# Kernel optimization log

Measured on AMD Instinct MI355X. Metric: run time of the kernel, lower is better.

Reference implementation:

```python
import math
import jax, jax.numpy as jnp
import numpy as np

NUM_HEADS = 32
NUM_KV_HEADS = 8
HEAD_SIZE = 128
FEATURE_DIM = 64
SEQ_LEN = 2048
WINDOW_SIZE = 64
EPS = 1e-12
MASK_VALUE = -100000000.0


def _make_masks(n: int, w: int):
    # block-diagonal ones(w,w) tiles, plus the rolled (sub-diagonal) tiles
    m = math.ceil(n / w)
    mask = np.kron(np.eye(m), np.ones((w, w)))
    mask = mask + np.roll(mask, -w, axis=-1)
    mask = mask[:n, :n]
    mask_window = np.tril(mask).astype(bool)[None, None]          # [1,1,n,n]
    mask_linear = np.tril(1.0 - mask).astype(bool)[None, None]    # [1,1,n,n]
    return jnp.asarray(mask_window), jnp.asarray(mask_linear)


def _feature_map(w, x):
    # f(x) = clamp(cat(softmax(xW), softmax(-xW)), min=eps)
    z = jnp.einsum('hdf,bhld->bhlf', w, x)
    return jnp.clip(
        jnp.concatenate([jax.nn.softmax(z, axis=-1), jax.nn.softmax(-z, axis=-1)], axis=-1),
        EPS, None)


def setup_inputs() -> dict:
    key = jax.random.key(0)
    ks = jax.random.split(key, 6)
    return {
        'query': jax.random.normal(ks[0], (SEQ_LEN, NUM_HEADS * HEAD_SIZE), dtype=jnp.float32),
        'key': jax.random.normal(ks[1], (SEQ_LEN, NUM_KV_HEADS * HEAD_SIZE), dtype=jnp.float32),
        'value': jax.random.normal(ks[2], (SEQ_LEN, NUM_KV_HEADS * HEAD_SIZE), dtype=jnp.float32),
        'fmap_q_w': 0.02 * jax.random.normal(ks[3], (NUM_HEADS, HEAD_SIZE, FEATURE_DIM), dtype=jnp.float32),
        'fmap_k_w': 0.02 * jax.random.normal(ks[4], (NUM_HEADS, HEAD_SIZE, FEATURE_DIM), dtype=jnp.float32),
        'window_factors': jax.random.normal(ks[5], (1, NUM_HEADS, 1, 1), dtype=jnp.float32),
    }


def reference(query, key, value, fmap_q_w, fmap_k_w, window_factors):
    T = query.shape[0]
    q = query.reshape(T, NUM_HEADS, HEAD_SIZE)
    k = key.reshape(T, NUM_KV_HEADS, HEAD_SIZE)
    v = value.reshape(T, NUM_KV_HEADS, HEAD_SIZE)
    rep = NUM_HEADS // NUM_KV_HEADS
    k = jnp.repeat(k, rep, axis=1)
    v = jnp.repeat(v, rep, axis=1)
    # [T,H,D] -> [1,H,T,D]
    q = jnp.moveaxis(q, 0, -2)[None]
    k = jnp.moveaxis(k, 0, -2)[None]
    v = jnp.moveaxis(v, 0, -2)[None]

    f_q = _feature_map(fmap_q_w, q)  # [1,H,T,2F]
    f_k = _feature_map(fmap_k_w, k)
    wf = jax.nn.sigmoid(window_factors)

    mask_window, mask_linear = _make_masks(SEQ_LEN, WINDOW_SIZE)
    mask_window = mask_window[:, :, :T, :T]
    mask_linear = mask_linear[:, :, :T, :T]

    # sliding-window softmax term
    a_sm = jnp.einsum('bhmd,bhnd->bhmn', q, k) * (HEAD_SIZE ** -0.5)
    a_sm = jnp.where(mask_window, a_sm, MASK_VALUE)
    a_sm_max = jnp.max(a_sm, axis=-1, keepdims=True)
    a_sm = wf * jnp.exp(a_sm - a_sm_max)
    sum_sm = jnp.sum(a_sm, axis=-1, keepdims=True)

    # linear feature-map term (linear_factor = 1)
    a_ln = jnp.einsum('bhmd,bhnd->bhmn', f_q, f_k)
    a_ln = jnp.where(mask_linear, a_ln, 0.0)
    sum_ln = jnp.sum(a_ln, axis=-1, keepdims=True)

    y = jnp.einsum('bhmn,bhnd->bhmd', a_sm + a_ln, v)
    return y / (sum_sm + sum_ln)
```

## Files before the change

kernel.cpp:

```cpp
#include <hip/hip_runtime.h>
#include <math.h>

#define T_SEQ 2048
#define NH    32
#define NKV   8
#define HS    128
#define FD    64
#define NBLK  32
#define SCAN_NB 30
#define EPSF  1e-12f
#define LDP   136
#define STP   129

typedef unsigned short u16;
typedef __bf16 bf16x8 __attribute__((ext_vector_type(8)));
typedef float  f32x4  __attribute__((ext_vector_type(4)));

__device__ __forceinline__ u16 f2b(float f) {
  unsigned u = __builtin_bit_cast(unsigned, f);
  return (u16)((u + 0x7fffu + ((u >> 16) & 1u)) >> 16);
}

#define FKT_OFF 0
#define ST_OFF  16777216
#define VT_OFF  54525952
#define WT_OFF  58720256
#define KB_OFF  59768832

__device__ __forceinline__ void stage_bf(u16* buf, const u16* __restrict__ src, int tid) {
#pragma unroll
  for (int i = 0; i < 4; ++i) {
    int idx = tid * 8 + i * 2048, rr = idx >> 7, c = idx & 127;
    *(uint4*)(buf + rr * LDP + c) = *(const uint4*)(src + idx);
  }
}
__device__ __forceinline__ void stage_vt(u16* buf, const u16* __restrict__ vts,
                                         int rofs, int kb0, int B, int tid) {
#pragma unroll
  for (int i = 0; i < 4; ++i) {
    int idx = tid * 8 + i * 2048, rr = idx >> 7, c = idx & 127;
    int key = (c < 64) ? (kb0 * 64 + c) : (B * 64 + (c - 64));
    *(uint4*)(buf + rr * LDP + c) = *(const uint4*)(vts + (size_t)(rr + rofs) * T_SEQ + key);
  }
}

__global__ __launch_bounds__(256) void k_pre(
    const float* __restrict__ wq, const float* __restrict__ wk,
    const float* __restrict__ vg,
    u16* __restrict__ WT, u16* __restrict__ VT)
{
  __shared__ float sB[128 * 68];
  const int bx = blockIdx.x, tid = threadIdx.x;

  if (bx < 64) {
    const int h = bx >> 1, isk = bx & 1;
    const float* src = (isk ? wk : wq) + (size_t)h * HS * FD;
    for (int idx = tid * 4; idx < 8192; idx += 1024) {
      int r = idx >> 6, c = idx & 63;
      *(float4*)(sB + r * 68 + c) = *(const float4*)(src + idx);
    }
    __syncthreads();
    u16* dst = WT + ((size_t)(isk * NH + h)) * 8192;
    for (int i = 0; i < 8; ++i) {
      int ch = tid + i * 256;
      int f = ch >> 5, d4 = (ch & 31) * 4;
      ushort4 u;
      u.x = f2b(sB[(d4 + 0) * 68 + f]);
      u.y = f2b(sB[(d4 + 1) * 68 + f]);
      u.z = f2b(sB[(d4 + 2) * 68 + f]);
      u.w = f2b(sB[(d4 + 3) * 68 + f]);
      *(ushort4*)(dst + f * 128 + d4) = u;
    }
  } else {
    const int idx2 = bx - 64;
    const int b = idx2 & 31, kvh = idx2 >> 5;
    float* sV = sB;
    for (int idx = tid * 4; idx < 8192; idx += 1024) {
      int r = idx >> 7, c = idx & 127;
      *(float4*)(sV + r * 129 + c) = *(const float4*)(vg + (size_t)(b * 64 + r) * (NKV * HS) + kvh * HS + c);
    }
    __syncthreads();
    const int lane = tid & 63, w = tid >> 6;
#pragma unroll
    for (int i = 0; i < 32; ++i) {
      int d = w * 32 + i;
      VT[((size_t)(kvh * 128 + d)) * T_SEQ + b * 64 + lane] = f2b(sV[lane * 129 + d]);
    }
  }
}

__global__ __launch_bounds__(256) void k_fmap(
    const float* __restrict__ kg, const u16* __restrict__ WT,
    u16* __restrict__ FKT, u16* __restrict__ KBB)
{
  __shared__ __align__(16) u16 smem[2 * 64 * 136];
  u16* sX = smem;
  u16* sW = smem + 64 * 136;
  const int lt = blockIdx.x, h = blockIdx.y;
  const int tid = threadIdx.x, lane = tid & 63, w = tid >> 6;
  const int quad = lane >> 4, txn = lane & 15;

  const float* xbase = kg + (h >> 2) * HS;
  const int    xstr  = NKV * HS;
  for (int idx = tid * 4; idx < 8192; idx += 1024) {
    int r = idx >> 7, c = idx & 127;
    float4 v4 = *(const float4*)(xbase + (size_t)(lt * 64 + r) * xstr + c);
    ushort4 u; u.x = f2b(v4.x); u.y = f2b(v4.y); u.z = f2b(v4.z); u.w = f2b(v4.w);
    *(ushort4*)(sX + r * 136 + c) = u;
  }
  const u16* wt = WT + ((size_t)(NH + h)) * 8192;
  for (int i = 0; i < 4; ++i) {
    int ch = tid + i * 256;
    int row = ch >> 4, d8 = (ch & 15) * 8;
    *(uint4*)(sW + row * 136 + d8) = *(const uint4*)(wt + row * 128 + d8);
  }
  __syncthreads();

  if ((h & 3) == 0) {
    u16* ob = KBB + ((size_t)((h >> 2) * NBLK + lt)) * 8192;
    for (int i = 0; i < 4; ++i) {
      int ch = tid + i * 256;
      int row = ch >> 4, d8 = (ch & 15) * 8;
      *(uint4*)(ob + row * 128 + d8) = *(const uint4*)(sX + row * 136 + d8);
    }
  }

  const int arow = w * 16 + txn;
  const f32x4 vzero = {0.f, 0.f, 0.f, 0.f};
  f32x4 zt[4] = {vzero, vzero, vzero, vzero};
#pragma unroll
  for (int ks = 0; ks < 4; ++ks) {
    bf16x8 a = *(const bf16x8*)(sX + arow * 136 + ks * 32 + quad * 8);
#pragma unroll
    for (int nt = 0; nt < 4; ++nt) {
      bf16x8 bb = *(const bf16x8*)(sW + (nt * 16 + txn) * 136 + ks * 32 + quad * 8);
      zt[nt] = __builtin_amdgcn_mfma_f32_16x16x32_bf16(a, bb, zt[nt], 0, 0, 0);
    }
  }

  float E1[4][4], E2[4][4];
#pragma unroll
  for (int r = 0; r < 4; ++r) {
    float zv[4];
    float mx = -1e30f, mn = 1e30f;
#pragma unroll
    for (int nt = 0; nt < 4; ++nt) {
      zv[nt] = zt[nt][r];
      mx = fmaxf(mx, zv[nt]); mn = fminf(mn, zv[nt]);
    }
#pragma unroll
    for (int o = 1; o < 16; o <<= 1) {
      mx = fmaxf(mx, __shfl_xor(mx, o));
      mn = fminf(mn, __shfl_xor(mn, o));
    }
    float e1[4], e2[4], s1 = 0.f, s2 = 0.f;
#pragma unroll
    for (int nt = 0; nt < 4; ++nt) {
      e1[nt] = __expf(zv[nt] - mx); s1 += e1[nt];
      e2[nt] = __expf(mn - zv[nt]); s2 += e2[nt];
    }
#pragma unroll
    for (int o = 1; o < 16; o <<= 1) { s1 += __shfl_xor(s1, o); s2 += __shfl_xor(s2, o); }
    float r1 = 1.f / s1, r2 = 1.f / s2;
#pragma unroll
    for (int nt = 0; nt < 4; ++nt) {
      E1[r][nt] = fmaxf(e1[nt] * r1, EPSF);
      E2[r][nt] = fmaxf(e2[nt] * r2, EPSF);
    }
  }

  __syncthreads();

#pragma unroll
  for (int r = 0; r < 4; ++r) {
    int j = w * 16 + quad * 4 + r;
#pragma unroll
    for (int nt = 0; nt < 4; ++nt) {
      sX[(nt * 16 + txn) * 68 + j]        = f2b(E1[r][nt]);
      sX[(nt * 16 + txn + 64) * 68 + j]   = f2b(E2[r][nt]);
    }
  }
  __syncthreads();
  u16* ob = FKT + (size_t)h * 128 * T_SEQ + lt * 64;
  for (int i = 0; i < 8; ++i) {
    int ch = tid + i * 256;
    int row = ch >> 4, j4 = (ch & 15) * 4;
    *(ushort4*)(ob + (size_t)row * T_SEQ + j4) = *(const ushort4*)(sX + row * 68 + j4);
  }
}

__global__ __launch_bounds__(256) void k_scan(
    const u16* __restrict__ FKT, const u16* __restrict__ VT, u16* __restrict__ ST)
{
  __shared__ __align__(16) u16 sVT[16 * 72];
  __shared__ __align__(16) u16 sFK[64 * 72];
  const int L = blockIdx.x + 8 * blockIdx.y + 16 * blockIdx.z;
  const int xcd = L & 7, j = L >> 3;
  const int hsub = j & 3, fh = (j >> 2) & 1, dc = j >> 3;
  const int h = xcd * 4 + hsub;
  const int tid = threadIdx.x, lane = tid & 63, w = tid >> 6;
  const int quad = lane >> 4, txn = lane & 15;
  const bool doz = (dc == 0);

  bf16x8 vone;
#pragma unroll
  for (int jj = 0; jj < 8; ++jj) vone[jj] = (__bf16)1.0f;

  const u16* vbase = VT + ((size_t)((h >> 2) * 128 + dc * 16)) * T_SEQ;
  const u16* fbase = FKT + ((size_t)(h * 128 + fh * 64)) * T_SEQ;

  const int srow = tid >> 4, sj4 = (tid & 15) * 4;
  ushort4 rv, rf[4];
  rv = *(const ushort4*)(vbase + (size_t)srow * T_SEQ + sj4);
#pragma unroll
  for (int i = 0; i < 4; ++i) {
    int ch = tid + i * 256;
    int fr = ch >> 4, fj4 = (ch & 15) * 4;
    rf[i] = *(const ushort4*)(fbase + (size_t)fr * T_SEQ + fj4);
  }

  const f32x4 vzero = {0.f, 0.f, 0.f, 0.f};
  f32x4 acc = vzero, zacc = vzero;

  for (int b = 0; b < SCAN_NB; ++b) {
    __syncthreads();
    *(ushort4*)(sVT + srow * 72 + sj4) = rv;
#pragma unroll
    for (int i = 0; i < 4; ++i) {
      int ch = tid + i * 256;
      int fr = ch >> 4, fj4 = (ch & 15) * 4;
      *(ushort4*)(sFK + fr * 72 + fj4) = rf[i];
    }
    __syncthreads();
    if (b + 1 < SCAN_NB) {
      rv = *(const ushort4*)(vbase + (size_t)srow * T_SEQ + (b + 1) * 64 + sj4);
#pragma unroll
      for (int i = 0; i < 4; ++i) {
        int ch = tid + i * 256;
        int fr = ch >> 4, fj4 = (ch & 15) * 4;
        rf[i] = *(const ushort4*)(fbase + (size_t)fr * T_SEQ + (b + 1) * 64 + fj4);
      }
    }
#pragma unroll
    for (int ks = 0; ks < 2; ++ks) {
      bf16x8 a  = *(const bf16x8*)(sVT + txn * 72 + ks * 32 + quad * 8);
      bf16x8 bb = *(const bf16x8*)(sFK + (w * 16 + txn) * 72 + ks * 32 + quad * 8);
      acc = __builtin_amdgcn_mfma_f32_16x16x32_bf16(a, bb, acc, 0, 0, 0);
      if (doz) zacc = __builtin_amdgcn_mfma_f32_16x16x32_bf16(vone, bb, zacc, 0, 0, 0);
    }
    u16* Sb = ST + (((size_t)(h * NBLK + b)) * STP + dc * 16) * 128 + fh * 64;
#pragma unroll
    for (int r = 0; r < 4; ++r)
      Sb[(quad * 4 + r) * 128 + w * 16 + txn] = f2b(acc[r]);
    if (doz && quad == 0)
      ST[(((size_t)(h * NBLK + b)) * STP + 128) * 128 + fh * 64 + w * 16 + txn] = f2b(zacc[0]);
  }
}

__global__ __launch_bounds__(256, 4) void k_main(
    const float* __restrict__ qg, const u16* __restrict__ KBB,
    const u16* __restrict__ WT, const u16* __restrict__ ST,
    const u16* __restrict__ VT, const float* __restrict__ wfac,
    float* __restrict__ out)
{
  __shared__ __align__(16) u16 RA[64 * LDP];
  __shared__ __align__(16) u16 RB[64 * LDP];
  __shared__ __align__(16) u16 sz[128];
  const int L = blockIdx.x + 32 * blockIdx.y;
  const int xcd = L & 7, j = L >> 3;
  const int hsub = j & 3, B = j >> 2;
  const int h = xcd * 4 + hsub;
  const int tid = threadIdx.x;
  const int lane = tid & 63, w = tid >> 6;
  const int quad = lane >> 4, txn = lane & 15;
  const int arow = w * 16 + txn;
  const int koff = quad * 8;

  const f32x4 vzero = {0.f, 0.f, 0.f, 0.f};
  f32x4 y[8];
#pragma unroll
  for (int t = 0; t < 8; ++t) y[t] = vzero;
  float sln[4] = {0.f, 0.f, 0.f, 0.f};
  const bf16x8 bzero = {0, 0, 0, 0, 0, 0, 0, 0};

  const int kb0 = (B >= 1) ? B - 1 : 0;
  const u16* ktB   = KBB + ((size_t)((h >> 2) * NBLK + B)) * 8192;
  const u16* ktP   = KBB + ((size_t)((h >> 2) * NBLK + kb0)) * 8192;
  const u16* vts   = VT  + (size_t)((h >> 2) * 128) * T_SEQ;

  for (int idx = tid * 4; idx < 8192; idx += 1024) {
    int r = idx >> 7, c = idx & 127;
    float4 v4 = *(const float4*)(qg + (size_t)(B * 64 + r) * (NH * HS) + h * HS + c);
    ushort4 u; u.x = f2b(v4.x); u.y = f2b(v4.y); u.z = f2b(v4.z); u.w = f2b(v4.w);
    *(ushort4*)(RA + r * LDP + c) = u;
  }
  if (B >= 2) stage_bf(RB, WT + (size_t)h * 8192, tid);
  __syncthreads();

  f32x4 zt[4] = {vzero, vzero, vzero, vzero};
  if (B >= 2) {
#pragma unroll
    for (int ks = 0; ks < 4; ++ks) {
      bf16x8 a = *(const bf16x8*)(RA + arow * LDP + ks * 32 + koff);
#pragma unroll
      for (int nt = 0; nt < 4; ++nt) {
        bf16x8 bb = *(const bf16x8*)(RB + (nt * 16 + txn) * LDP + ks * 32 + koff);
        zt[nt] = __builtin_amdgcn_mfma_f32_16x16x32_bf16(a, bb, zt[nt], 0, 0, 0);
      }
    }
  }
  __syncthreads();
  stage_bf(RB, ktB, tid);

  unsigned Epk[4][4];
  if (B >= 2) {
#pragma unroll
    for (int r = 0; r < 4; ++r) {
      float zv[4];
      float mx = -1e30f, mn = 1e30f;
#pragma unroll
      for (int nt = 0; nt < 4; ++nt) {
        zv[nt] = zt[nt][r];
        mx = fmaxf(mx, zv[nt]); mn = fminf(mn, zv[nt]);
      }
#pragma unroll
      for (int o = 1; o < 16; o <<= 1) {
        mx = fmaxf(mx, __shfl_xor(mx, o));
        mn = fminf(mn, __shfl_xor(mn, o));
      }
      float e1[4], e2[4], s1 = 0.f, s2 = 0.f;
#pragma unroll
      for (int nt = 0; nt < 4; ++nt) {
        e1[nt] = __expf(zv[nt] - mx); s1 += e1[nt];
        e2[nt] = __expf(mn - zv[nt]); s2 += e2[nt];
      }
#pragma unroll
      for (int o = 1; o < 16; o <<= 1) { s1 += __shfl_xor(s1, o); s2 += __shfl_xor(s2, o); }
      float r1 = 1.f / s1, r2 = 1.f / s2;
#pragma unroll
      for (int nt = 0; nt < 4; ++nt) {
        unsigned lo = f2b(fmaxf(e1[nt] * r1, EPSF));
        unsigned hi = f2b(fmaxf(e2[nt] * r2, EPSF));
        Epk[r][nt] = lo | (hi << 16);
      }
    }
  }
  __syncthreads();

  f32x4 s[8];
#pragma unroll
  for (int t = 0; t < 8; ++t) s[t] = vzero;
#pragma unroll
  for (int ks = 0; ks < 4; ++ks) {
    bf16x8 a = *(const bf16x8*)(RA + arow * LDP + ks * 32 + koff);
#pragma unroll
    for (int t = 0; t < 4; ++t) {
      bf16x8 bb = *(const bf16x8*)(RB + (t * 16 + txn) * LDP + ks * 32 + koff);
      s[4 + t] = __builtin_amdgcn_mfma_f32_16x16x32_bf16(a, bb, s[4 + t], 0, 0, 0);
    }
  }

  if (B >= 1) {
    __syncthreads();
    stage_bf(RB, ktP, tid);
    __syncthreads();
#pragma unroll
    for (int ks = 0; ks < 4; ++ks) {
      bf16x8 a = *(const bf16x8*)(RA + arow * LDP + ks * 32 + koff);
#pragma unroll
      for (int t = 0; t < 4; ++t) {
        bf16x8 bb = *(const bf16x8*)(RB + (t * 16 + txn) * LDP + ks * 32 + koff);
        s[t] = __builtin_amdgcn_mfma_f32_16x16x32_bf16(a, bb, s[t], 0, 0, 0);
      }
    }
  }

  float wf = wfac[h];
  wf = 1.f / (1.f + __expf(-wf));
  const float scale = 0.08838834764831845f;
  float ssum[4];
#pragma unroll
  for (int r = 0; r < 4; ++r) {
    const int irow = w * 16 + quad * 4 + r;
    float sv[8];
    float m = -1e30f;
#pragma unroll
    for (int t = 0; t < 8; ++t) {
      float x = s[t][r] * scale;
      bool msk = (t < 4) ? (B == 0) : ((t - 4) * 16 + txn > irow);
      x = msk ? -1e30f : x;
      sv[t] = x;
      m = fmaxf(m, x);
    }
#pragma unroll
    for (int o = 1; o < 16; o <<= 1) m = fmaxf(m, __shfl_xor(m, o));
    float ss = 0.f;
#pragma unroll
    for (int t = 0; t < 8; ++t) {
      float e = (sv[t] > -1e29f) ? wf * __expf(sv[t] - m) : 0.f;
      ss += e;
      RA[irow * LDP + t * 16 + txn] = f2b(e);
    }
#pragma unroll
    for (int o = 1; o < 16; o <<= 1) ss += __shfl_xor(ss, o);
    ssum[r] = ss;
  }
  __syncthreads();

  stage_vt(RB, vts, 0, kb0, B, tid);
  __syncthreads();
#pragma unroll
  for (int ks = 0; ks < 4; ++ks) {
    if (B == 0 && ks < 2) continue;
    bf16x8 a = *(const bf16x8*)(RA + arow * LDP + ks * 32 + koff);
#pragma unroll
    for (int t = 0; t < 4; ++t) {
      bf16x8 bb = *(const bf16x8*)(RB + (t * 16 + txn) * LDP + ks * 32 + koff);
      y[t] = __builtin_amdgcn_mfma_f32_16x16x32_bf16(a, bb, y[t], 0, 0, 0);
    }
  }
  __syncthreads();

  stage_vt(RB, vts, 64, kb0, B, tid);
  __syncthreads();
#pragma unroll
  for (int ks = 0; ks < 4; ++ks) {
    if (B == 0 && ks < 2) continue;
    bf16x8 a = *(const bf16x8*)(RA + arow * LDP + ks * 32 + koff);
#pragma unroll
    for (int t = 4; t < 8; ++t) {
      bf16x8 bb = *(const bf16x8*)(RB + (t * 16 + txn - 64) * LDP + ks * 32 + koff);
      y[t] = __builtin_amdgcn_mfma_f32_16x16x32_bf16(a, bb, y[t], 0, 0, 0);
    }
  }

  if (B >= 2) {
    __syncthreads();
#pragma unroll
    for (int r = 0; r < 4; ++r) {
      int row = w * 16 + quad * 4 + r;
#pragma unroll
      for (int nt = 0; nt < 4; ++nt) {
        RA[row * LDP + nt * 16 + txn]      = (u16)(Epk[r][nt] & 0xffffu);
        RA[row * LDP + 64 + nt * 16 + txn] = (u16)(Epk[r][nt] >> 16);
      }
    }
    const u16* ssrc = ST + ((size_t)(h * NBLK + (B - 2))) * (STP * 128);
    stage_bf(RB, ssrc, tid);
    if (tid < 32) *(ushort4*)(sz + tid * 4) = *(const ushort4*)(ssrc + 16384 + tid * 4);
    __syncthreads();
    f32x4 yz = vzero;
#pragma unroll
    for (int ks = 0; ks < 4; ++ks) {
      bf16x8 a = *(const bf16x8*)(RA + arow * LDP + ks * 32 + koff);
#pragma unroll
      for (int t = 0; t < 4; ++t) {
        bf16x8 bb = *(const bf16x8*)(RB + (t * 16 + txn) * LDP + ks * 32 + koff);
        y[t] = __builtin_amdgcn_mfma_f32_16x16x32_bf16(a, bb, y[t], 0, 0, 0);
      }
      bf16x8 bz = (txn == 0) ? *(const bf16x8*)(sz + ks * 32 + koff) : bzero;
      yz = __builtin_amdgcn_mfma_f32_16x16x32_bf16(a, bz, yz, 0, 0, 0);
    }
    __syncthreads();
    stage_bf(RB, ssrc + 8192, tid);
    __syncthreads();
#pragma unroll
    for (int ks = 0; ks < 4; ++ks) {
      bf16x8 a = *(const bf16x8*)(RA + arow * LDP + ks * 32 + koff);
#pragma unroll
      for (int t = 4; t < 8; ++t) {
        bf16x8 bb = *(const bf16x8*)(RB + (t * 16 + txn - 64) * LDP + ks * 32 + koff);
        y[t] = __builtin_amdgcn_mfma_f32_16x16x32_bf16(a, bb, y[t], 0, 0, 0);
      }
    }
#pragma unroll
    for (int r = 0; r < 4; ++r) sln[r] = __shfl(yz[r], lane & 48);
  }

  const size_t obase = ((size_t)h * T_SEQ + B * 64) * HS;
#pragma unroll
  for (int r = 0; r < 4; ++r) {
    float inv = 1.f / (ssum[r] + sln[r]);
    int irow = w * 16 + quad * 4 + r;
#pragma unroll
    for (int t = 0; t < 8; ++t)
      out[obase + (size_t)irow * HS + t * 16 + txn] = y[t][r] * inv;
  }
}

extern "C" void kernel_launch(void* const* d_in, const int* in_sizes, int n_in,
                              void* d_out, int out_size, void* d_ws, size_t ws_size,
                              hipStream_t stream) {
  const float* q    = (const float*)d_in[0];
  const float* k    = (const float*)d_in[1];
  const float* v    = (const float*)d_in[2];
  const float* wq   = (const float*)d_in[3];
  const float* wk   = (const float*)d_in[4];
  const float* wfac = (const float*)d_in[5];
  float* out = (float*)d_out;
  char* wsb = (char*)d_ws;

  u16* FKT = (u16*)(wsb + FKT_OFF);
  u16* ST  = (u16*)(wsb + ST_OFF);
  u16* VT  = (u16*)(wsb + VT_OFF);
  u16* WT  = (u16*)(wsb + WT_OFF);
  u16* KBB = (u16*)(wsb + KB_OFF);

  k_pre  <<<dim3(320),      256, 0, stream>>>(wq, wk, v, WT, VT);
  k_fmap <<<dim3(NBLK, NH), 256, 0, stream>>>(k, WT, FKT, KBB);
  k_scan <<<dim3(8, 2, NH), 256, 0, stream>>>(FKT, VT, ST);
  k_main <<<dim3(NBLK, NH), 256, 0, stream>>>(q, KBB, WT, ST, VT, wfac, out);
}
```

Before: 161.5 us.

## Load MFMA operands directly from global memory, dropping LDS staging and barriers

k_main and k_scan now read the B operands (K blocks, W, V transposes, scan states) directly from global/L2 into MFMA fragments instead of staging them through shared memory behind __syncthreads. Each wave converts its own Q rows into LDS, which removes the block-wide barriers before the first MFMAs. The V transpose moves from k_pre into the k_fmap launch, so k_pre now only handles the weights. The goal is less LDS traffic and fewer barriers, at the cost of redundant, less coalesced global loads across waves.

Measured after the change: 193.2 us. 19.6% more time.

```diff
diff --git a/kernel.cpp b/kernel.cpp
--- a/kernel.cpp
+++ b/kernel.cpp
@@ -27,78 +27,62 @@
 #define WT_OFF  58720256
 #define KB_OFF  59768832
 
-__device__ __forceinline__ void stage_bf(u16* buf, const u16* __restrict__ src, int tid) {
-#pragma unroll
-  for (int i = 0; i < 4; ++i) {
-    int idx = tid * 8 + i * 2048, rr = idx >> 7, c = idx & 127;
-    *(uint4*)(buf + rr * LDP + c) = *(const uint4*)(src + idx);
-  }
-}
-__device__ __forceinline__ void stage_vt(u16* buf, const u16* __restrict__ vts,
-                                         int rofs, int kb0, int B, int tid) {
-#pragma unroll
-  for (int i = 0; i < 4; ++i) {
-    int idx = tid * 8 + i * 2048, rr = idx >> 7, c = idx & 127;
-    int key = (c < 64) ? (kb0 * 64 + c) : (B * 64 + (c - 64));
-    *(uint4*)(buf + rr * LDP + c) = *(const uint4*)(vts + (size_t)(rr + rofs) * T_SEQ + key);
-  }
-}
-
 __global__ __launch_bounds__(256) void k_pre(
     const float* __restrict__ wq, const float* __restrict__ wk,
-    const float* __restrict__ vg,
-    u16* __restrict__ WT, u16* __restrict__ VT)
+    u16* __restrict__ WT)
 {
   __shared__ float sB[128 * 68];
   const int bx = blockIdx.x, tid = threadIdx.x;
-
-  if (bx < 64) {
-    const int h = bx >> 1, isk = bx & 1;
-    const float* src = (isk ? wk : wq) + (size_t)h * HS * FD;
-    for (int idx = tid * 4; idx < 8192; idx += 1024) {
-      int r = idx >> 6, c = idx & 63;
-      *(float4*)(sB + r * 68 + c) = *(const float4*)(src + idx);
-    }
-    __syncthreads();
-    u16* dst = WT + ((size_t)(isk * NH + h)) * 8192;
-    for (int i = 0; i < 8; ++i) {
-      int ch = tid + i * 256;
-      int f = ch >> 5, d4 = (ch & 31) * 4;
-      ushort4 u;
-      u.x = f2b(sB[(d4 + 0) * 68 + f]);
-      u.y = f2b(sB[(d4 + 1) * 68 + f]);
-      u.z = f2b(sB[(d4 + 2) * 68 + f]);
-      u.w = f2b(sB[(d4 + 3) * 68 + f]);
-      *(ushort4*)(dst + f * 128 + d4) = u;
-    }
-  } else {
-    const int idx2 = bx - 64;
-    const int b = idx2 & 31, kvh = idx2 >> 5;
-    float* sV = sB;
+  const int h = bx >> 1, isk = bx & 1;
+  const float* src = (isk ? wk : wq) + (size_t)h * HS * FD;
+  for (int idx = tid * 4; idx < 8192; idx += 1024) {
+    int r = idx >> 6, c = idx & 63;
+    *(float4*)(sB + r * 68 + c) = *(const float4*)(src + idx);
+  }
+  __syncthreads();
+  u16* dst = WT + ((size_t)(isk * NH + h)) * 8192;
+  for (int i = 0; i < 8; ++i) {
+    int ch = tid + i * 256;
+    int f = ch >> 5, d4 = (ch & 31) * 4;
+    ushort4 u;
+    u.x = f2b(sB[(d4 + 0) * 68 + f]);
+    u.y = f2b(sB[(d4 + 1) * 68 + f]);
+    u.z = f2b(sB[(d4 + 2) * 68 + f]);
+    u.w = f2b(sB[(d4 + 3) * 68 + f]);
+    *(ushort4*)(dst + f * 128 + d4) = u;
+  }
+}
+
+__global__ __launch_bounds__(256) void k_fmap(
+    const float* __restrict__ kg, const float* __restrict__ vg,
+    const u16* __restrict__ WT,
+    u16* __restrict__ FKT, u16* __restrict__ KBB, u16* __restrict__ VT)
+{
+  __shared__ __align__(16) u16 smem[2 * 64 * 136];
+  const int bx = blockIdx.x;
+  const int tid = threadIdx.x, lane = tid & 63, w = tid >> 6;
+  const int quad = lane >> 4, txn = lane & 15;
+
+  if (bx < 256) {
+    const int b = bx & 31, kvh = bx >> 5;
+    float* sV = (float*)smem;
     for (int idx = tid * 4; idx < 8192; idx += 1024) {
       int r = idx >> 7, c = idx & 127;
       *(float4*)(sV + r * 129 + c) = *(const float4*)(vg + (size_t)(b * 64 + r) * (NKV * HS) + kvh * HS + c);
     }
     __syncthreads();
-    const int lane = tid & 63, w = tid >> 6;
 #pragma unroll
     for (int i = 0; i < 32; ++i) {
       int d = w * 32 + i;
       VT[((size_t)(kvh * 128 + d)) * T_SEQ + b * 64 + lane] = f2b(sV[lane * 129 + d]);
     }
-  }
-}
-
-__global__ __launch_bounds__(256) void k_fmap(
-    const float* __restrict__ kg, const u16* __restrict__ WT,
-    u16* __restrict__ FKT, u16* __restrict__ KBB)
-{
-  __shared__ __align__(16) u16 smem[2 * 64 * 136];
+    return;
+  }
+
+  const int id = bx - 256;
+  const int lt = id & 31, h = id >> 5;
   u16* sX = smem;
   u16* sW = smem + 64 * 136;
-  const int lt = blockIdx.x, h = blockIdx.y;
-  const int tid = threadIdx.x, lane = tid & 63, w = tid >> 6;
-  const int quad = lane >> 4, txn = lane & 15;
 
   const float* xbase = kg + (h >> 2) * HS;
   const int    xstr  = NKV * HS;
@@ -192,8 +176,6 @@
 __global__ __launch_bounds__(256) void k_scan(
     const u16* __restrict__ FKT, const u16* __restrict__ VT, u16* __restrict__ ST)
 {
-  __shared__ __align__(16) u16 sVT[16 * 72];
-  __shared__ __align__(16) u16 sFK[64 * 72];
   const int L = blockIdx.x + 8 * blockIdx.y + 16 * blockIdx.z;
   const int xcd = L & 7, j = L >> 3;
   const int hsub = j & 3, fh = (j >> 2) & 1, dc = j >> 3;
@@ -206,47 +188,24 @@
 #pragma unroll
   for (int jj = 0; jj < 8; ++jj) vone[jj] = (__bf16)1.0f;
 
-  const u16* vbase = VT + ((size_t)((h >> 2) * 128 + dc * 16)) * T_SEQ;
-  const u16* fbase = FKT + ((size_t)(h * 128 + fh * 64)) * T_SEQ;
-
-  const int srow = tid >> 4, sj4 = (tid & 15) * 4;
-  ushort4 rv, rf[4];
-  rv = *(const ushort4*)(vbase + (size_t)srow * T_SEQ + sj4);
-#pragma unroll
-  for (int i = 0; i < 4; ++i) {
-    int ch = tid + i * 256;
-    int fr = ch >> 4, fj4 = (ch & 15) * 4;
-    rf[i] = *(const ushort4*)(fbase + (size_t)fr * T_SEQ + fj4);
-  }
+  const u16* va = VT  + ((size_t)((h >> 2) * 128 + dc * 16 + txn)) * T_SEQ + quad * 8;
+  const u16* fa = FKT + ((size_t)(h * 128 + fh * 64 + w * 16 + txn)) * T_SEQ + quad * 8;
 
   const f32x4 vzero = {0.f, 0.f, 0.f, 0.f};
   f32x4 acc = vzero, zacc = vzero;
 
+#pragma unroll 2
   for (int b = 0; b < SCAN_NB; ++b) {
-    __syncthreads();
-    *(ushort4*)(sVT + srow * 72 + sj4) = rv;
-#pragma unroll
-    for (int i = 0; i < 4; ++i) {
-      int ch = tid + i * 256;
-      int fr = ch >> 4, fj4 = (ch & 15) * 4;
-      *(ushort4*)(sFK + fr * 72 + fj4) = rf[i];
-    }
-    __syncthreads();
-    if (b + 1 < SCAN_NB) {
-      rv = *(const ushort4*)(vbase + (size_t)srow * T_SEQ + (b + 1) * 64 + sj4);
-#pragma unroll
-      for (int i = 0; i < 4; ++i) {
-        int ch = tid + i * 256;
-        int fr = ch >> 4, fj4 = (ch & 15) * 4;
-        rf[i] = *(const ushort4*)(fbase + (size_t)fr * T_SEQ + (b + 1) * 64 + fj4);
-      }
-    }
-#pragma unroll
-    for (int ks = 0; ks < 2; ++ks) {
-      bf16x8 a  = *(const bf16x8*)(sVT + txn * 72 + ks * 32 + quad * 8);
-      bf16x8 bb = *(const bf16x8*)(sFK + (w * 16 + txn) * 72 + ks * 32 + quad * 8);
-      acc = __builtin_amdgcn_mfma_f32_16x16x32_bf16(a, bb, acc, 0, 0, 0);
-      if (doz) zacc = __builtin_amdgcn_mfma_f32_16x16x32_bf16(vone, bb, zacc, 0, 0, 0);
+    const int c0 = b * 64;
+    bf16x8 a0  = *(const bf16x8*)(va + c0);
+    bf16x8 b0  = *(const bf16x8*)(fa + c0);
+    bf16x8 a1  = *(const bf16x8*)(va + c0 + 32);
+    bf16x8 b1  = *(const bf16x8*)(fa + c0 + 32);
+    acc = __builtin_amdgcn_mfma_f32_16x16x32_bf16(a0, b0, acc, 0, 0, 0);
+    acc = __builtin_amdgcn_mfma_f32_16x16x32_bf16(a1, b1, acc, 0, 0, 0);
+    if (doz) {
+      zacc = __builtin_amdgcn_mfma_f32_16x16x32_bf16(vone, b0, zacc, 0, 0, 0);
+      zacc = __builtin_amdgcn_mfma_f32_16x16x32_bf16(vone, b1, zacc, 0, 0, 0);
     }
     u16* Sb = ST + (((size_t)(h * NBLK + b)) * STP + dc * 16) * 128 + fh * 64;
 #pragma unroll
@@ -264,11 +223,9 @@
     float* __restrict__ out)
 {
   __shared__ __align__(16) u16 RA[64 * LDP];
-  __shared__ __align__(16) u16 RB[64 * LDP];
-  __shared__ __align__(16) u16 sz[128];
   const int L = blockIdx.x + 32 * blockIdx.y;
-  const int xcd = L & 7, j = L >> 3;
-  const int hsub = j & 3, B = j >> 2;
+  const int xcd = L & 7, jj = L >> 3;
+  const int hsub = jj & 3, B = jj >> 2;
   const int h = xcd * 4 + hsub;
   const int tid = threadIdx.x;
   const int lane = tid & 63, w = tid >> 6;
@@ -284,18 +241,23 @@
   const bf16x8 bzero = {0, 0, 0, 0, 0, 0, 0, 0};
 
   const int kb0 = (B >= 1) ? B - 1 : 0;
-  const u16* ktB   = KBB + ((size_t)((h >> 2) * NBLK + B)) * 8192;
-  const u16* ktP   = KBB + ((size_t)((h >> 2) * NBLK + kb0)) * 8192;
-  const u16* vts   = VT  + (size_t)((h >> 2) * 128) * T_SEQ;
-
-  for (int idx = tid * 4; idx < 8192; idx += 1024) {
-    int r = idx >> 7, c = idx & 127;
-    float4 v4 = *(const float4*)(qg + (size_t)(B * 64 + r) * (NH * HS) + h * HS + c);
-    ushort4 u; u.x = f2b(v4.x); u.y = f2b(v4.y); u.z = f2b(v4.z); u.w = f2b(v4.w);
-    *(ushort4*)(RA + r * LDP + c) = u;
-  }
-  if (B >= 2) stage_bf(RB, WT + (size_t)h * 8192, tid);
-  __syncthreads();
+  const u16* ktB = KBB + ((size_t)((h >> 2) * NBLK + B)) * 8192;
+  const u16* ktP = KBB + ((size_t)((h >> 2) * NBLK + kb0)) * 8192;
+  const u16* vts = VT  + (size_t)((h >> 2) * 128) * T_SEQ;
+  const u16* wqt = WT  + (size_t)h * 8192;
+  const u16* ssrc = ST + ((size_t)(h * NBLK + (B >= 2 ? B - 2 : 0))) * (STP * 128);
+
+  {
+    const float* qb = qg + (size_t)(B * 64 + w * 16) * (NH * HS) + h * HS;
+#pragma unroll
+    for (int i = 0; i < 8; ++i) {
+      int idx = lane + i * 64;
+      int r = idx >> 5, c4 = (idx & 31) * 4;
+      float4 v4 = *(const float4*)(qb + (size_t)r * (NH * HS) + c4);
+      ushort4 u; u.x = f2b(v4.x); u.y = f2b(v4.y); u.z = f2b(v4.z); u.w = f2b(v4.w);
+      *(ushort4*)(RA + (w * 16 + r) * LDP + c4) = u;
+    }
+  }
 
   f32x4 zt[4] = {vzero, vzero, vzero, vzero};
   if (B >= 2) {
@@ -304,13 +266,11 @@
       bf16x8 a = *(const bf16x8*)(RA + arow * LDP + ks * 32 + koff);
 #pragma unroll
       for (int nt = 0; nt < 4; ++nt) {
-        bf16x8 bb = *(const bf16x8*)(RB + (nt * 16 + txn) * LDP + ks * 32 + koff);
+        bf16x8 bb = *(const bf16x8*)(wqt + (nt * 16 + txn) * 128 + ks * 32 + koff);
         zt[nt] = __builtin_amdgcn_mfma_f32_16x16x32_bf16(a, bb, zt[nt], 0, 0, 0);
       }
     }
   }
-  __syncthreads();
-  stage_bf(RB, ktB, tid);
 
   unsigned Epk[4][4];
   if (B >= 2) {
@@ -345,7 +305,6 @@
       }
     }
   }
-  __syncthreads();
 
   f32x4 s[8];
 #pragma unroll
@@ -355,21 +314,17 @@
     bf16x8 a = *(const bf16x8*)(RA + arow * LDP + ks * 32 + koff);
 #pragma unroll
     for (int t = 0; t < 4; ++t) {
-      bf16x8 bb = *(const bf16x8*)(RB + (t * 16 + txn) * LDP + ks * 32 + koff);
+      bf16x8 bb = *(const bf16x8*)(ktB + (t * 16 + txn) * 128 + ks * 32 + koff);
       s[4 + t] = __builtin_amdgcn_mfma_f32_16x16x32_bf16(a, bb, s[4 + t], 0, 0, 0);
     }
   }
-
   if (B >= 1) {
-    __syncthreads();
-    stage_bf(RB, ktP, tid);
-    __syncthreads();
 #pragma unroll
     for (int ks = 0; ks < 4; ++ks) {
       bf16x8 a = *(const bf16x8*)(RA + arow * LDP + ks * 32 + koff);
 #pragma unroll
       for (int t = 0; t < 4; ++t) {
-        bf16x8 bb = *(const bf16x8*)(RB + (t * 16 + txn) * LDP + ks * 32 + koff);
+        bf16x8 bb = *(const bf16x8*)(ktP + (t * 16 + txn) * 128 + ks * 32 + koff);
         s[t] = __builtin_amdgcn_mfma_f32_16x16x32_bf16(a, bb, s[t], 0, 0, 0);
       }
     }
@@ -405,37 +360,20 @@
     for (int o = 1; o < 16; o <<= 1) ss += __shfl_xor(ss, o);
     ssum[r] = ss;
   }
-  __syncthreads();
-
-  stage_vt(RB, vts, 0, kb0, B, tid);
-  __syncthreads();
+
 #pragma unroll
   for (int ks = 0; ks < 4; ++ks) {
     if (B == 0 && ks < 2) continue;
+    const int kcol = (ks < 2) ? (kb0 * 64 + ks * 32) : (B * 64 + (ks - 2) * 32);
     bf16x8 a = *(const bf16x8*)(RA + arow * LDP + ks * 32 + koff);
 #pragma unroll
-    for (int t = 0; t < 4; ++t) {
-      bf16x8 bb = *(const bf16x8*)(RB + (t * 16 + txn) * LDP + ks * 32 + koff);
+    for (int t = 0; t < 8; ++t) {
+      bf16x8 bb = *(const bf16x8*)(vts + (size_t)(t * 16 + txn) * T_SEQ + kcol + koff);
       y[t] = __builtin_amdgcn_mfma_f32_16x16x32_bf16(a, bb, y[t], 0, 0, 0);
     }
   }
-  __syncthreads();
-
-  stage_vt(RB, vts, 64, kb0, B, tid);
-  __syncthreads();
-#pragma unroll
-  for (int ks = 0; ks < 4; ++ks) {
-    if (B == 0 && ks < 2) continue;
-    bf16x8 a = *(const bf16x8*)(RA + arow * LDP + ks * 32 + koff);
-#pragma unroll
-    for (int t = 4; t < 8; ++t) {
-      bf16x8 bb = *(const bf16x8*)(RB + (t * 16 + txn - 64) * LDP + ks * 32 + koff);
-      y[t] = __builtin_amdgcn_mfma_f32_16x16x32_bf16(a, bb, y[t], 0, 0, 0);
-    }
-  }
 
   if (B >= 2) {
-    __syncthreads();
 #pragma unroll
     for (int r = 0; r < 4; ++r) {
       int row = w * 16 + quad * 4 + r;
@@ -445,33 +383,17 @@
         RA[row * LDP + 64 + nt * 16 + txn] = (u16)(Epk[r][nt] >> 16);
       }
     }
-    const u16* ssrc = ST + ((size_t)(h * NBLK + (B - 2))) * (STP * 128);
-    stage_bf(RB, ssrc, tid);
-    if (tid < 32) *(ushort4*)(sz + tid * 4) = *(const ushort4*)(ssrc + 16384 + tid * 4);
-    __syncthreads();
     f32x4 yz = vzero;
 #pragma unroll
     for (int ks = 0; ks < 4; ++ks) {
       bf16x8 a = *(const bf16x8*)(RA + arow * LDP + ks * 32 + koff);
 #pragma unroll
-      for (int t = 0; t < 4; ++t) {
-        bf16x8 bb = *(const bf16x8*)(RB + (t * 16 + txn) * LDP + ks * 32 + koff);
+      for (int t = 0; t < 8; ++t) {
+        bf16x8 bb = *(const bf16x8*)(ssrc + (t * 16 + txn) * 128 + ks * 32 + koff);
         y[t] = __builtin_amdgcn_mfma_f32_16x16x32_bf16(a, bb, y[t], 0, 0, 0);
       }
-      bf16x8 bz = (txn == 0) ? *(const bf16x8*)(sz + ks * 32 + koff) : bzero;
+      bf16x8 bz = (txn == 0) ? *(const bf16x8*)(ssrc + 16384 + ks * 32 + koff) : bzero;
       yz = __builtin_amdgcn_mfma_f32_16x16x32_bf16(a, bz, yz, 0, 0, 0);
-    }
-    __syncthreads();
-    stage_bf(RB, ssrc + 8192, tid);
-    __syncthreads();
-#pragma unroll
-    for (int ks = 0; ks < 4; ++ks) {
-      bf16x8 a = *(const bf16x8*)(RA + arow * LDP + ks * 32 + koff);
-#pragma unroll
-      for (int t = 4; t < 8; ++t) {
-        bf16x8 bb = *(const bf16x8*)(RB + (t * 16 + txn - 64) * LDP + ks * 32 + koff);
-        y[t] = __builtin_amdgcn_mfma_f32_16x16x32_bf16(a, bb, y[t], 0, 0, 0);
-      }
     }
 #pragma unroll
     for (int r = 0; r < 4; ++r) sln[r] = __shfl(yz[r], lane & 48);
@@ -506,8 +428,8 @@
   u16* WT  = (u16*)(wsb + WT_OFF);
   u16* KBB = (u16*)(wsb + KB_OFF);
 
-  k_pre  <<<dim3(320),      256, 0, stream>>>(wq, wk, v, WT, VT);
-  k_fmap <<<dim3(NBLK, NH), 256, 0, stream>>>(k, WT, FKT, KBB);
+  k_pre  <<<dim3(64),       256, 0, stream>>>(wq, wk, WT);
+  k_fmap <<<dim3(1280),     256, 0, stream>>>(k, v, WT, FKT, KBB, VT);
   k_scan <<<dim3(8, 2, NH), 256, 0, stream>>>(FKT, VT, ST);
   k_main <<<dim3(NBLK, NH), 256, 0, stream>>>(q, KBB, WT, ST, VT, wfac, out);
 }
```

## Software-pipeline global tile loads through registers and use lighter barriers in k_main

Applied to the files above, without the earlier changes.

Restructures k_main so that each global tile (K blocks, V^T halves, state halves) is loaded into registers one stage ahead and written to shared memory after the next barrier, overlapping global latency with the MFMA work. The W^T feature-map weights are now read directly from global memory instead of being staged, and each wave converts only its own Q rows, which removes the first barriers. __syncthreads is replaced with raw s_barrier, plus lgkmcnt waits where shared writes must be visible. The cost is higher register pressure from the prefetch buffer, and B<2 blocks now perform unconditional state-tile loads and barriers.

Result: slower. 165.3 us (+2.3%).

```diff
diff --git a/kernel.cpp b/kernel.cpp
--- a/kernel.cpp
+++ b/kernel.cpp
@@ -21,26 +21,37 @@
   return (u16)((u + 0x7fffu + ((u >> 16) & 1u)) >> 16);
 }
 
+__device__ __forceinline__ void bar() {
+  asm volatile("s_barrier" ::: "memory");
+}
+__device__ __forceinline__ void bar_lgkm() {
+  asm volatile("s_waitcnt lgkmcnt(0)\n\ts_barrier" ::: "memory");
+}
+
 #define FKT_OFF 0
 #define ST_OFF  16777216
 #define VT_OFF  54525952
 #define WT_OFF  58720256
 #define KB_OFF  59768832
 
-__device__ __forceinline__ void stage_bf(u16* buf, const u16* __restrict__ src, int tid) {
-#pragma unroll
-  for (int i = 0; i < 4; ++i) {
-    int idx = tid * 8 + i * 2048, rr = idx >> 7, c = idx & 127;
-    *(uint4*)(buf + rr * LDP + c) = *(const uint4*)(src + idx);
-  }
-}
-__device__ __forceinline__ void stage_vt(u16* buf, const u16* __restrict__ vts,
-                                         int rofs, int kb0, int B, int tid) {
+__device__ __forceinline__ void ld_tile(uint4 p[4], const u16* __restrict__ src, int tid) {
+#pragma unroll
+  for (int i = 0; i < 4; ++i) p[i] = *(const uint4*)(src + tid * 8 + i * 2048);
+}
+__device__ __forceinline__ void ld_vt(uint4 p[4], const u16* __restrict__ vts,
+                                      int rofs, int kb0, int B, int tid) {
 #pragma unroll
   for (int i = 0; i < 4; ++i) {
     int idx = tid * 8 + i * 2048, rr = idx >> 7, c = idx & 127;
     int key = (c < 64) ? (kb0 * 64 + c) : (B * 64 + (c - 64));
-    *(uint4*)(buf + rr * LDP + c) = *(const uint4*)(vts + (size_t)(rr + rofs) * T_SEQ + key);
+    p[i] = *(const uint4*)(vts + (size_t)(rr + rofs) * T_SEQ + key);
+  }
+}
+__device__ __forceinline__ void wr_tile(u16* buf, int tid, const uint4 p[4]) {
+#pragma unroll
+  for (int i = 0; i < 4; ++i) {
+    int idx = tid * 8 + i * 2048, rr = idx >> 7, c = idx & 127;
+    *(uint4*)(buf + rr * LDP + c) = p[i];
   }
 }
 
@@ -223,7 +234,7 @@
   f32x4 acc = vzero, zacc = vzero;
 
   for (int b = 0; b < SCAN_NB; ++b) {
-    __syncthreads();
+    bar();
     *(ushort4*)(sVT + srow * 72 + sj4) = rv;
 #pragma unroll
     for (int i = 0; i < 4; ++i) {
@@ -231,7 +242,7 @@
       int fr = ch >> 4, fj4 = (ch & 15) * 4;
       *(ushort4*)(sFK + fr * 72 + fj4) = rf[i];
     }
-    __syncthreads();
+    bar_lgkm();
     if (b + 1 < SCAN_NB) {
       rv = *(const ushort4*)(vbase + (size_t)srow * T_SEQ + (b + 1) * 64 + sj4);
 #pragma unroll
@@ -267,8 +278,8 @@
   __shared__ __align__(16) u16 RB[64 * LDP];
   __shared__ __align__(16) u16 sz[128];
   const int L = blockIdx.x + 32 * blockIdx.y;
-  const int xcd = L & 7, j = L >> 3;
-  const int hsub = j & 3, B = j >> 2;
+  const int xcd = L & 7, jj = L >> 3;
+  const int hsub = jj & 3, B = jj >> 2;
   const int h = xcd * 4 + hsub;
   const int tid = threadIdx.x;
   const int lane = tid & 63, w = tid >> 6;
@@ -284,18 +295,26 @@
   const bf16x8 bzero = {0, 0, 0, 0, 0, 0, 0, 0};
 
   const int kb0 = (B >= 1) ? B - 1 : 0;
-  const u16* ktB   = KBB + ((size_t)((h >> 2) * NBLK + B)) * 8192;
-  const u16* ktP   = KBB + ((size_t)((h >> 2) * NBLK + kb0)) * 8192;
-  const u16* vts   = VT  + (size_t)((h >> 2) * 128) * T_SEQ;
-
-  for (int idx = tid * 4; idx < 8192; idx += 1024) {
-    int r = idx >> 7, c = idx & 127;
-    float4 v4 = *(const float4*)(qg + (size_t)(B * 64 + r) * (NH * HS) + h * HS + c);
-    ushort4 u; u.x = f2b(v4.x); u.y = f2b(v4.y); u.z = f2b(v4.z); u.w = f2b(v4.w);
-    *(ushort4*)(RA + r * LDP + c) = u;
-  }
-  if (B >= 2) stage_bf(RB, WT + (size_t)h * 8192, tid);
-  __syncthreads();
+  const u16* ktB = KBB + ((size_t)((h >> 2) * NBLK + B)) * 8192;
+  const u16* ktP = KBB + ((size_t)((h >> 2) * NBLK + kb0)) * 8192;
+  const u16* vts = VT  + (size_t)((h >> 2) * 128) * T_SEQ;
+  const u16* wqt = WT  + (size_t)h * 8192;
+  const u16* ssrc = ST + ((size_t)(h * NBLK + (B >= 2 ? B - 2 : 0))) * (STP * 128);
+
+  uint4 pf[4];
+  ld_tile(pf, ktB, tid);
+
+  {
+    const float* qb = qg + (size_t)(B * 64 + w * 16) * (NH * HS) + h * HS;
+#pragma unroll
+    for (int i = 0; i < 8; ++i) {
+      int idx = lane + i * 64;
+      int r = idx >> 5, c4 = (idx & 31) * 4;
+      float4 v4 = *(const float4*)(qb + (size_t)r * (NH * HS) + c4);
+      ushort4 u; u.x = f2b(v4.x); u.y = f2b(v4.y); u.z = f2b(v4.z); u.w = f2b(v4.w);
+      *(ushort4*)(RA + (w * 16 + r) * LDP + c4) = u;
+    }
+  }
 
   f32x4 zt[4] = {vzero, vzero, vzero, vzero};
   if (B >= 2) {
@@ -304,13 +323,11 @@
       bf16x8 a = *(const bf16x8*)(RA + arow * LDP + ks * 32 + koff);
 #pragma unroll
       for (int nt = 0; nt < 4; ++nt) {
-        bf16x8 bb = *(const bf16x8*)(RB + (nt * 16 + txn) * LDP + ks * 32 + koff);
+        bf16x8 bb = *(const bf16x8*)(wqt + (nt * 16 + txn) * 128 + ks * 32 + koff);
         zt[nt] = __builtin_amdgcn_mfma_f32_16x16x32_bf16(a, bb, zt[nt], 0, 0, 0);
       }
     }
   }
-  __syncthreads();
-  stage_bf(RB, ktB, tid);
 
   unsigned Epk[4][4];
   if (B >= 2) {
@@ -345,7 +362,10 @@
       }
     }
   }
-  __syncthreads();
+
+  wr_tile(RB, tid, pf);
+  ld_tile(pf, ktP, tid);
+  bar_lgkm();
 
   f32x4 s[8];
 #pragma unroll
@@ -359,11 +379,12 @@
       s[4 + t] = __builtin_amdgcn_mfma_f32_16x16x32_bf16(a, bb, s[4 + t], 0, 0, 0);
     }
   }
-
+  bar();
+
+  wr_tile(RB, tid, pf);
+  ld_vt(pf, vts, 0, kb0, B, tid);
+  bar_lgkm();
   if (B >= 1) {
-    __syncthreads();
-    stage_bf(RB, ktP, tid);
-    __syncthreads();
 #pragma unroll
     for (int ks = 0; ks < 4; ++ks) {
       bf16x8 a = *(const bf16x8*)(RA + arow * LDP + ks * 32 + koff);
@@ -405,10 +426,13 @@
     for (int o = 1; o < 16; o <<= 1) ss += __shfl_xor(ss, o);
     ssum[r] = ss;
   }
-  __syncthreads();
-
-  stage_vt(RB, vts, 0, kb0, B, tid);
-  __syncthreads();
+  bar();
+
+  wr_tile(RB, tid, pf);
+  ld_vt(pf, vts, 64, kb0, B, tid);
+  ushort4 zz = {0, 0, 0, 0};
+  if (tid < 32) zz = *(const ushort4*)(ssrc + 16384 + tid * 4);
+  bar_lgkm();
 #pragma unroll
   for (int ks = 0; ks < 4; ++ks) {
     if (B == 0 && ks < 2) continue;
@@ -419,10 +443,11 @@
       y[t] = __builtin_amdgcn_mfma_f32_16x16x32_bf16(a, bb, y[t], 0, 0, 0);
     }
   }
-  __syncthreads();
-
-  stage_vt(RB, vts, 64, kb0, B, tid);
-  __syncthreads();
+  bar();
+
+  wr_tile(RB, tid, pf);
+  ld_tile(pf, ssrc, tid);
+  bar_lgkm();
 #pragma unroll
   for (int ks = 0; ks < 4; ++ks) {
     if (B == 0 && ks < 2) continue;
@@ -433,9 +458,7 @@
       y[t] = __builtin_amdgcn_mfma_f32_16x16x32_bf16(a, bb, y[t], 0, 0, 0);
     }
   }
-
   if (B >= 2) {
-    __syncthreads();
 #pragma unroll
     for (int r = 0; r < 4; ++r) {
       int row = w * 16 + quad * 4 + r;
@@ -445,11 +468,15 @@
         RA[row * LDP + 64 + nt * 16 + txn] = (u16)(Epk[r][nt] >> 16);
       }
     }
-    const u16* ssrc = ST + ((size_t)(h * NBLK + (B - 2))) * (STP * 128);
-    stage_bf(RB, ssrc, tid);
-    if (tid < 32) *(ushort4*)(sz + tid * 4) = *(const ushort4*)(ssrc + 16384 + tid * 4);
-    __syncthreads();
-    f32x4 yz = vzero;
+  }
+  bar();
+
+  wr_tile(RB, tid, pf);
+  if (tid < 32) *(ushort4*)(sz + tid * 4) = zz;
+  ld_tile(pf, ssrc + 8192, tid);
+  bar_lgkm();
+  f32x4 yz = vzero;
+  if (B >= 2) {
 #pragma unroll
     for (int ks = 0; ks < 4; ++ks) {
       bf16x8 a = *(const bf16x8*)(RA + arow * LDP + ks * 32 + koff);
@@ -461,9 +488,12 @@
       bf16x8 bz = (txn == 0) ? *(const bf16x8*)(sz + ks * 32 + koff) : bzero;
       yz = __builtin_amdgcn_mfma_f32_16x16x32_bf16(a, bz, yz, 0, 0, 0);
     }
-    __syncthreads();
-    stage_bf(RB, ssrc + 8192, tid);
-    __syncthreads();
+  }
+  bar();
+
+  wr_tile(RB, tid, pf);
+  bar_lgkm();
+  if (B >= 2) {
 #pragma unroll
     for (int ks = 0; ks < 4; ++ks) {
       bf16x8 a = *(const bf16x8*)(RA + arow * LDP + ks * 32 + koff);
```
